# Kernel tuning notes

Hardware: AMD Instinct MI355X
Metric: run time of the kernel (lower is better)

Reference implementation:

```python
import jax, jax.numpy as jnp
import numpy as np

N_BITS = 4
GROUP_SIZE = 128
CLIP_RATIO = 1.0  # no clipping when == 1.0
EPS = 1e-5


def setup_inputs() -> dict:
    key = jax.random.key(0)
    k1, k2 = jax.random.split(key)
    B, S, C = 4, 4096, 4096
    x = jax.random.normal(k1, (B, S, C), dtype=jnp.float32)
    perm = jax.random.permutation(k2, C).astype(jnp.int32)
    inv = jnp.argsort(perm).astype(jnp.int32)
    return {"x": x, "perm_indices": perm, "inverse_perm_indices": inv}


def _quantize_groupwise(w):
    """Asymmetric int quant/dequant, quant_method='max', per flat group of GROUP_SIZE."""
    saved_shape = w.shape
    g = w.reshape(-1, GROUP_SIZE)  # [num_groups, group_size]
    q_max = 2 ** N_BITS - 1  # asym: q_min = 0
    w_max = jnp.max(g, axis=-1, keepdims=True)
    w_min = jnp.min(g, axis=-1, keepdims=True)
    scales = jnp.clip(w_max - w_min, EPS, None) / q_max
    base = jnp.clip(jnp.round(-w_min / scales), 0, q_max)
    q = (jnp.clip(jnp.round(g / scales) + base, 0, q_max) - base) * scales
    return q.reshape(saved_shape)


def reference(x, perm_indices, inverse_perm_indices):
    # cluster-based channel permutation -> group-wise quant/dequant -> inverse permutation
    x_perm = jnp.take(x, perm_indices, axis=-1)
    x_q = _quantize_groupwise(x_perm)
    return jnp.take(x_q, inverse_perm_indices, axis=-1)
```

## Files before the change

kernel.cpp:

```cpp
#include <hip/hip_runtime.h>


constexpr int C       = 4096;
constexpr int GS      = 128;
constexpr int NGROUPS = C / GS;
constexpr int BLOCK   = 256;
constexpr int WAVES   = BLOCK / 64;
constexpr int GPW     = NGROUPS / WAVES;
constexpr int VECS    = C / 4 / BLOCK;

__global__ __launch_bounds__(BLOCK) void tpq_kernel(
    const float* __restrict__ x,
    const int*   __restrict__ gat,
    const int*   __restrict__ asn,
    float*       __restrict__ out,
    int rows)
{
    __shared__ float row[C];
    __shared__ float sc[NGROUPS];
    __shared__ float bs[NGROUPS];

    const int wave = threadIdx.x >> 6;
    const int lane = threadIdx.x & 63;

    for (int r = blockIdx.x; r < rows; r += gridDim.x) {
        const float4* xr4 = reinterpret_cast<const float4*>(x + (size_t)r * C);
        const int4*   as4 = reinterpret_cast<const int4*>(asn);
        float4*       or4 = reinterpret_cast<float4*>(out + (size_t)r * C);
        float4*       rw4 = reinterpret_cast<float4*>(row);

        #pragma unroll
        for (int i = 0; i < VECS; ++i)
            rw4[threadIdx.x + i * BLOCK] = xr4[threadIdx.x + i * BLOCK];
        __syncthreads();

        #pragma unroll
        for (int gi = 0; gi < GPW; ++gi) {
            const int g  = wave * GPW + gi;
            const int j0 = g * GS + lane;
            const float v0 = row[gat[j0]];
            const float v1 = row[gat[j0 + 64]];
            float mx = fmaxf(v0, v1);
            float mn = fminf(v0, v1);
            #pragma unroll
            for (int off = 32; off > 0; off >>= 1) {
                mx = fmaxf(mx, __shfl_xor(mx, off));
                mn = fminf(mn, __shfl_xor(mn, off));
            }
            if (lane == 0) {
                const float scale = fmaxf(mx - mn, 1e-5f) * (1.0f / 15.0f);
                const float base  = fminf(fmaxf(rintf(-mn / scale), 0.0f), 15.0f);
                sc[g] = scale;
                bs[g] = base;
            }
        }
        __syncthreads();

        #pragma unroll
        for (int i = 0; i < VECS; ++i) {
            const int idx = threadIdx.x + i * BLOCK;
            const int4   gidx = as4[idx];
            const float4 v    = rw4[idx];
            float4 o;
            {
                const float s = sc[gidx.x >> 7], b = bs[gidx.x >> 7];
                o.x = (fminf(fmaxf(rintf(v.x / s) + b, 0.0f), 15.0f) - b) * s;
            }
            {
                const float s = sc[gidx.y >> 7], b = bs[gidx.y >> 7];
                o.y = (fminf(fmaxf(rintf(v.y / s) + b, 0.0f), 15.0f) - b) * s;
            }
            {
                const float s = sc[gidx.z >> 7], b = bs[gidx.z >> 7];
                o.z = (fminf(fmaxf(rintf(v.z / s) + b, 0.0f), 15.0f) - b) * s;
            }
            {
                const float s = sc[gidx.w >> 7], b = bs[gidx.w >> 7];
                o.w = (fminf(fmaxf(rintf(v.w / s) + b, 0.0f), 15.0f) - b) * s;
            }
            or4[idx] = o;
        }
        __syncthreads();
    }
}

extern "C" void kernel_launch(void* const* d_in, const int* in_sizes, int n_in,
                              void* d_out, int out_size, void* d_ws, size_t ws_size,
                              hipStream_t stream) {
    const float* x = (const float*)d_in[0];
    const int* gat = (const int*)d_in[1];
    const int* asn = (const int*)d_in[2];
    float* out = (float*)d_out;

    const int rows = in_sizes[0] / C;
    const int nblk = rows < 2048 ? rows : 2048;

    tpq_kernel<<<nblk, BLOCK, 0, stream>>>(x, gat, asn, out, rows);
}
```

Measured before the change: 125.5 us.

## Double-buffer rows via async global-to-LDS loads and hoist permutation indices

Each row is now staged into one of two LDS buffers with global_load_lds, so the next row's load is issued while the current row is quantized. The gather and assignment indices are loaded once per block into registers, with group ids packed into bytes, instead of being re-read from global memory every row. The block size grows to 512 threads, scale and base are stored as one float2, and the trailing barrier is dropped. In exchange, LDS use per block doubles and register pressure rises from the hoisted index arrays.

```diff
diff --git a/kernel.cpp b/kernel.cpp
--- a/kernel.cpp
+++ b/kernel.cpp
@@ -1,95 +1,119 @@
 #include <hip/hip_runtime.h>
+#include <stdint.h>
 
 
-constexpr int C       = 4096;
-constexpr int GS      = 128;
-constexpr int NGROUPS = C / GS;
-constexpr int BLOCK   = 256;
-constexpr int WAVES   = BLOCK / 64;
-constexpr int GPW     = NGROUPS / WAVES;
-constexpr int VECS    = C / 4 / BLOCK;
+constexpr int C     = 4096;
+constexpr int GS    = 128;
+constexpr int NG    = C / GS;
+constexpr int BLOCK = 512;
+constexpr int WAVES = BLOCK / 64;
+constexpr int GPW   = NG / WAVES;
+constexpr int VECS  = C / 4 / BLOCK;
 
-__global__ __launch_bounds__(BLOCK) void tpq_kernel(
+typedef const __attribute__((address_space(1))) uint32_t glb_u32;
+typedef __attribute__((address_space(3))) uint32_t lds_u32;
+
+__device__ __forceinline__ void stage_row(const float* __restrict__ src,
+                                          float* dst, int wave, int lane) {
+    #pragma unroll
+    for (int i = 0; i < 2; ++i) {
+        const float* g = src + i * 2048 + wave * 256 + lane * 4;
+        float*       l = dst + i * 2048 + wave * 256;
+        __builtin_amdgcn_global_load_lds((glb_u32*)(uintptr_t)g,
+                                         (lds_u32*)(uintptr_t)l, 16, 0, 0);
+    }
+}
+
+__global__ __launch_bounds__(BLOCK, 8) void tpq_kernel(
     const float* __restrict__ x,
     const int*   __restrict__ gat,
     const int*   __restrict__ asn,
     float*       __restrict__ out,
     int rows)
 {
-    __shared__ float row[C];
-    __shared__ float sc[NGROUPS];
-    __shared__ float bs[NGROUPS];
+    __shared__ float  rowbuf[2][C];
+    __shared__ float2 sb[NG];
 
-    const int wave = threadIdx.x >> 6;
-    const int lane = threadIdx.x & 63;
+    const int tid  = threadIdx.x;
+    const int wave = tid >> 6;
+    const int lane = tid & 63;
 
-    for (int r = blockIdx.x; r < rows; r += gridDim.x) {
-        const float4* xr4 = reinterpret_cast<const float4*>(x + (size_t)r * C);
-        const int4*   as4 = reinterpret_cast<const int4*>(asn);
-        float4*       or4 = reinterpret_cast<float4*>(out + (size_t)r * C);
-        float4*       rw4 = reinterpret_cast<float4*>(row);
+    int pidx0[GPW], pidx1[GPW];
+    #pragma unroll
+    for (int gi = 0; gi < GPW; ++gi) {
+        const int g = wave * GPW + gi;
+        pidx0[gi] = gat[g * GS + lane];
+        pidx1[gi] = gat[g * GS + 64 + lane];
+    }
+    uint32_t gpack[VECS];
+    #pragma unroll
+    for (int i = 0; i < VECS; ++i) {
+        const int4 a = reinterpret_cast<const int4*>(asn)[tid + i * BLOCK];
+        gpack[i] = (uint32_t)(a.x >> 7)        | ((uint32_t)(a.y >> 7) << 8)
+                 | ((uint32_t)(a.z >> 7) << 16) | ((uint32_t)(a.w >> 7) << 24);
+    }
 
-        #pragma unroll
-        for (int i = 0; i < VECS; ++i)
-            rw4[threadIdx.x + i * BLOCK] = xr4[threadIdx.x + i * BLOCK];
+    int r = blockIdx.x;
+    if (r >= rows) return;
+    stage_row(x + (size_t)r * C, rowbuf[0], wave, lane);
+    int cur = 0;
+
+    while (true) {
         __syncthreads();
+        const int  rn = r + gridDim.x;
+        const bool hn = rn < rows;
+        if (hn) stage_row(x + (size_t)rn * C, rowbuf[cur ^ 1], wave, lane);
 
+        const float* rc = rowbuf[cur];
         #pragma unroll
         for (int gi = 0; gi < GPW; ++gi) {
-            const int g  = wave * GPW + gi;
-            const int j0 = g * GS + lane;
-            const float v0 = row[gat[j0]];
-            const float v1 = row[gat[j0 + 64]];
+            const float v0 = rc[pidx0[gi]];
+            const float v1 = rc[pidx1[gi]];
             float mx = fmaxf(v0, v1);
             float mn = fminf(v0, v1);
             #pragma unroll
-            for (int off = 32; off > 0; off >>= 1) {
+            for (int off = 32; off; off >>= 1) {
                 mx = fmaxf(mx, __shfl_xor(mx, off));
                 mn = fminf(mn, __shfl_xor(mn, off));
             }
             if (lane == 0) {
-                const float scale = fmaxf(mx - mn, 1e-5f) * (1.0f / 15.0f);
-                const float base  = fminf(fmaxf(rintf(-mn / scale), 0.0f), 15.0f);
-                sc[g] = scale;
-                bs[g] = base;
+                const float s = fmaxf(mx - mn, 1e-5f) * (1.0f / 15.0f);
+                const float b = fminf(fmaxf(rintf(-mn / s), 0.0f), 15.0f);
+                sb[wave * GPW + gi] = make_float2(s, b);
             }
         }
         __syncthreads();
 
+        const float4* rc4 = reinterpret_cast<const float4*>(rc);
+        float4*       or4 = reinterpret_cast<float4*>(out + (size_t)r * C);
         #pragma unroll
         for (int i = 0; i < VECS; ++i) {
-            const int idx = threadIdx.x + i * BLOCK;
-            const int4   gidx = as4[idx];
-            const float4 v    = rw4[idx];
+            const float4   v  = rc4[tid + i * BLOCK];
+            const uint32_t gp = gpack[i];
             float4 o;
-            {
-                const float s = sc[gidx.x >> 7], b = bs[gidx.x >> 7];
-                o.x = (fminf(fmaxf(rintf(v.x / s) + b, 0.0f), 15.0f) - b) * s;
-            }
-            {
-                const float s = sc[gidx.y >> 7], b = bs[gidx.y >> 7];
-                o.y = (fminf(fmaxf(rintf(v.y / s) + b, 0.0f), 15.0f) - b) * s;
-            }
-            {
-                const float s = sc[gidx.z >> 7], b = bs[gidx.z >> 7];
-                o.z = (fminf(fmaxf(rintf(v.z / s) + b, 0.0f), 15.0f) - b) * s;
-            }
-            {
-                const float s = sc[gidx.w >> 7], b = bs[gidx.w >> 7];
-                o.w = (fminf(fmaxf(rintf(v.w / s) + b, 0.0f), 15.0f) - b) * s;
-            }
-            or4[idx] = o;
+            { const float2 p = sb[gp & 31u];
+              o.x = (fminf(fmaxf(rintf(v.x / p.x) + p.y, 0.0f), 15.0f) - p.y) * p.x; }
+            { const float2 p = sb[(gp >> 8) & 31u];
+              o.y = (fminf(fmaxf(rintf(v.y / p.x) + p.y, 0.0f), 15.0f) - p.y) * p.x; }
+            { const float2 p = sb[(gp >> 16) & 31u];
+              o.z = (fminf(fmaxf(rintf(v.z / p.x) + p.y, 0.0f), 15.0f) - p.y) * p.x; }
+            { const float2 p = sb[(gp >> 24) & 31u];
+              o.w = (fminf(fmaxf(rintf(v.w / p.x) + p.y, 0.0f), 15.0f) - p.y) * p.x; }
+            or4[tid + i * BLOCK] = o;
         }
-        __syncthreads();
+
+        if (!hn) break;
+        r = rn;
+        cur ^= 1;
     }
 }
 
 extern "C" void kernel_launch(void* const* d_in, const int* in_sizes, int n_in,
                               void* d_out, int out_size, void* d_ws, size_t ws_size,
                               hipStream_t stream) {
-    const float* x = (const float*)d_in[0];
-    const int* gat = (const int*)d_in[1];
-    const int* asn = (const int*)d_in[2];
+    const float* x   = (const float*)d_in[0];
+    const int*   gat = (const int*)d_in[1];
+    const int*   asn = (const int*)d_in[2];
     float* out = (float*)d_out;
 
     const int rows = in_sizes[0] / C;
```

Result: faster. 118.7 us (-5.4%).
